# Kernel optimization log

Hardware: AMD Instinct MI355X
Metric: run time of the kernel (lower is better)

The kernel has to match this reference:

```python
import jax, jax.numpy as jnp
import numpy as np
from jax import lax

B, C_IN, C_OUT, N, R, K = 16, 64, 64, 32768, 32, 3
GROUPS, GN_EPS = 8, 1e-5


def swish(x):
    return x * jax.nn.sigmoid(x)


def group_norm(x, gamma, beta):
    b, c = x.shape[:2]
    xg = x.reshape(b, GROUPS, -1)
    mu = xg.mean(-1, keepdims=True)
    var = xg.var(-1, keepdims=True)
    xn = ((xg - mu) * lax.rsqrt(var + GN_EPS)).reshape(x.shape)
    shp = (1, c) + (1,) * (x.ndim - 2)
    return xn * gamma.reshape(shp) + beta.reshape(shp)


def conv3d(x, w, b):
    y = lax.conv_general_dilated(x, w, (1, 1, 1), 'SAME',
                                 dimension_numbers=('NCDHW', 'OIDHW', 'NCDHW'))
    return y + b.reshape(1, -1, 1, 1, 1)


def voxelize(features, coords):
    # features [B,C,N], coords [B,3,N] -> vox [B,C,R,R,R], norm_coords [B,3,N] in [0,R-1]
    c = coords - coords.mean(axis=2, keepdims=True)
    scale = jnp.linalg.norm(c, axis=1, keepdims=True).max(axis=2, keepdims=True) * 2.0  # eps=0
    norm = jnp.clip((c / scale + 0.5) * R, 0.0, R - 1)
    vc = jnp.round(norm).astype(jnp.int32)
    idx = (vc[:, 0] * R + vc[:, 1]) * R + vc[:, 2]  # [B,N] flat voxel index

    def per_batch(f, i):  # f [C,N], i [N] -> [C, R^3] scatter-average
        sums = jax.ops.segment_sum(f.T, i, num_segments=R ** 3)  # [R^3, C]
        cnt = jax.ops.segment_sum(jnp.ones(i.shape, f.dtype), i, num_segments=R ** 3)
        return (sums / jnp.maximum(cnt, 1.0)[:, None]).T

    vox = jax.vmap(per_batch)(features, idx).reshape(features.shape[0], features.shape[1], R, R, R)
    return vox, norm


def trilinear_devoxelize(vox, coords):
    # vox [B,C,R,R,R], coords [B,3,N] float in [0,R-1] -> [B,C,N]
    b, c = vox.shape[:2]
    flat = vox.reshape(b, c, R ** 3)
    c0f = jnp.floor(coords)
    f = coords - c0f
    i0 = jnp.clip(c0f.astype(jnp.int32), 0, R - 1)
    i1 = jnp.clip(i0 + 1, 0, R - 1)
    out = jnp.zeros((b, c, coords.shape[2]), vox.dtype)
    for xi, wx in ((i0[:, 0], 1.0 - f[:, 0]), (i1[:, 0], f[:, 0])):
        for yi, wy in ((i0[:, 1], 1.0 - f[:, 1]), (i1[:, 1], f[:, 1])):
            for zi, wz in ((i0[:, 2], 1.0 - f[:, 2]), (i1[:, 2], f[:, 2])):
                idx = (xi * R + yi) * R + zi  # [B,N]
                w = (wx * wy * wz)[:, None, :]
                out = out + jnp.take_along_axis(flat, idx[:, None, :], axis=2) * w
    return out


def setup_inputs():
    key = jax.random.key(0)
    ks = jax.random.split(key, 6)
    s1 = 1.0 / np.sqrt(C_IN * K ** 3)
    s2 = 1.0 / np.sqrt(C_OUT * K ** 3)
    sp = 1.0 / np.sqrt(C_IN)
    return {
        'features': jax.random.normal(ks[0], (B, C_IN, N), jnp.float32),
        'coords': jax.random.normal(ks[1], (B, 3, N), jnp.float32),
        'w1': jax.random.normal(ks[2], (C_OUT, C_IN, K, K, K), jnp.float32) * s1,
        'b1': jnp.zeros((C_OUT,), jnp.float32),
        'g1': jnp.ones((C_OUT,), jnp.float32),
        'be1': jnp.zeros((C_OUT,), jnp.float32),
        'w2': jax.random.normal(ks[3], (C_OUT, C_OUT, K, K, K), jnp.float32) * s2,
        'b2': jnp.zeros((C_OUT,), jnp.float32),
        'g2': jnp.ones((C_OUT,), jnp.float32),
        'be2': jnp.zeros((C_OUT,), jnp.float32),
        'wp': jax.random.normal(ks[4], (C_OUT, C_IN), jnp.float32) * sp,
        'bp': jnp.zeros((C_OUT,), jnp.float32),
        'gp': jnp.ones((C_OUT,), jnp.float32),
        'bep': jnp.zeros((C_OUT,), jnp.float32),
    }


def reference(features, coords, w1, b1, g1, be1, w2, b2, g2, be2, wp, bp, gp, bep):
    coords_sg = lax.stop_gradient(coords)  # torch: coords.detach() inside Voxelization
    vox, norm_coords = voxelize(features, coords_sg)
    h = swish(group_norm(conv3d(vox, w1, b1), g1, be1))
    # Dropout(0.1) is identity in eval mode
    h = swish(group_norm(conv3d(h, w2, b2), g2, be2))
    vpts = trilinear_devoxelize(h, norm_coords)
    pf = swish(group_norm(jnp.einsum('oc,bcn->bon', wp, features) + bp[None, :, None], gp, bep))
    return (vpts + pf, coords)
```

## Files before the change

kernel.cpp:

```cpp
#include <hip/hip_runtime.h>
#include <hip/hip_bf16.h>
#include <math.h>

#define BB   16
#define CCH  64
#define NPT  32768
#define RR   32
#define R3   32768
#define GSZ  262144
#define VOXB 2228224

typedef __attribute__((ext_vector_type(8))) short bfx8;
typedef __attribute__((ext_vector_type(8))) unsigned short usx8;
typedef __attribute__((ext_vector_type(16))) float f32x16;

__device__ __forceinline__ short f2bf(float f) {
    unsigned u = __builtin_bit_cast(unsigned, f);
    u += 0x7fff + ((u >> 16) & 1);
    return (short)(u >> 16);
}
__device__ __forceinline__ float bf2f(unsigned short s) {
    unsigned u = ((unsigned)s) << 16;
    return __builtin_bit_cast(float, u);
}

__device__ __forceinline__ int fzswz(int z) {
    return (((z & 3) ^ ((z >> 2) & 3)) << 3);
}

__device__ __forceinline__ float blockReduceSumF(float v) {
    __shared__ float sm[16];
    #pragma unroll
    for (int o = 32; o > 0; o >>= 1) v += __shfl_down(v, o);
    __syncthreads();
    if ((threadIdx.x & 63) == 0) sm[threadIdx.x >> 6] = v;
    __syncthreads();
    float s = 0.f;
    int nw = blockDim.x >> 6;
    for (int i = 0; i < nw; ++i) s += sm[i];
    return s;
}

__device__ __forceinline__ float blockReduceMaxF(float v) {
    __shared__ float sm[16];
    #pragma unroll
    for (int o = 32; o > 0; o >>= 1) v = fmaxf(v, __shfl_down(v, o));
    __syncthreads();
    if ((threadIdx.x & 63) == 0) sm[threadIdx.x >> 6] = v;
    __syncthreads();
    float s = sm[0];
    int nw = blockDim.x >> 6;
    for (int i = 1; i < nw; ++i) s = fmaxf(s, sm[i]);
    return s;
}

__global__ void k_cstat_sum(const float* __restrict__ coords, float* __restrict__ csum) {
    int b = blockIdx.x >> 3, seg = blockIdx.x & 7;
    const float* cb = coords + (size_t)b * 3 * NPT;
    int n0 = seg << 12;
    float sx = 0.f, sy = 0.f, sz = 0.f;
    for (int n = n0 + threadIdx.x; n < n0 + 4096; n += 256) {
        sx += cb[n]; sy += cb[NPT + n]; sz += cb[2 * NPT + n];
    }
    sx = blockReduceSumF(sx);
    sy = blockReduceSumF(sy);
    sz = blockReduceSumF(sz);
    if (threadIdx.x == 0) {
        atomicAdd(&csum[b * 4 + 0], sx);
        atomicAdd(&csum[b * 4 + 1], sy);
        atomicAdd(&csum[b * 4 + 2], sz);
    }
}

__global__ void k_cstat_max(const float* __restrict__ coords, const float* __restrict__ csum,
                            int* __restrict__ cmax) {
    int b = blockIdx.x >> 3, seg = blockIdx.x & 7;
    const float* cb = coords + (size_t)b * 3 * NPT;
    float mx = csum[b * 4 + 0] * (1.f / NPT);
    float my = csum[b * 4 + 1] * (1.f / NPT);
    float mz = csum[b * 4 + 2] * (1.f / NPT);
    int n0 = seg << 12;
    float mn = 0.f;
    for (int n = n0 + threadIdx.x; n < n0 + 4096; n += 256) {
        float x = cb[n] - mx, y = cb[NPT + n] - my, z = cb[2 * NPT + n] - mz;
        mn = fmaxf(mn, sqrtf(x * x + y * y + z * z));
    }
    mn = blockReduceMaxF(mn);
    if (threadIdx.x == 0) atomicMax(&cmax[b], __float_as_int(mn));
}

__global__ void k_norm_idx(const float* __restrict__ coords, const float* __restrict__ csum,
                           const int* __restrict__ cmax,
                           float* __restrict__ normc, int* __restrict__ vidx,
                           int* __restrict__ hist, float* __restrict__ out2) {
    int t = blockIdx.x * 256 + threadIdx.x;
    int b = t >> 15, n = t & 32767;
    float mx = csum[b * 4 + 0] * (1.f / NPT);
    float my = csum[b * 4 + 1] * (1.f / NPT);
    float mz = csum[b * 4 + 2] * (1.f / NPT);
    float scale = 2.f * __int_as_float(cmax[b]);
    const float* cb = coords + (size_t)b * 3 * NPT;
    float x = cb[n], y = cb[NPT + n], z = cb[2 * NPT + n];
    float nx = fminf(fmaxf(((x - mx) / scale + 0.5f) * 32.f, 0.f), 31.f);
    float ny = fminf(fmaxf(((y - my) / scale + 0.5f) * 32.f, 0.f), 31.f);
    float nz = fminf(fmaxf(((z - mz) / scale + 0.5f) * 32.f, 0.f), 31.f);
    float* nb = normc + (size_t)b * 3 * NPT;
    nb[n] = nx; nb[NPT + n] = ny; nb[2 * NPT + n] = nz;
    int vx = (int)rintf(nx), vy = (int)rintf(ny), vz = (int)rintf(nz);
    int v = (vx * 32 + vy) * 32 + vz;
    vidx[t] = v;
    atomicAdd(&hist[(b << 15) + v], 1);
    float* o2 = out2 + (size_t)b * 3 * NPT;
    o2[n] = x; o2[NPT + n] = y; o2[2 * NPT + n] = z;
}

__global__ __launch_bounds__(1024) void k_prefix(const int* __restrict__ hist,
                                                 int* __restrict__ startB,
                                                 int* __restrict__ base) {
    int b = blockIdx.x;
    int tid = threadIdx.x;
    const int* h = hist + (b << 15);
    int loc[32];
    int s = 0;
    #pragma unroll
    for (int j = 0; j < 32; ++j) { loc[j] = h[tid * 32 + j]; s += loc[j]; }
    __shared__ int sm[1024];
    sm[tid] = s;
    __syncthreads();
    for (int o = 1; o < 1024; o <<= 1) {
        int v = (tid >= o) ? sm[tid - o] : 0;
        __syncthreads();
        sm[tid] += v;
        __syncthreads();
    }
    int run = (tid ? sm[tid - 1] : 0);
    #pragma unroll
    for (int j = 0; j < 32; ++j) {
        int idx = (b << 15) + tid * 32 + j;
        startB[idx] = run;
        base[idx] = run;
        run += loc[j];
    }
}

__global__ __launch_bounds__(256) void k_reorder(const float* __restrict__ feat,
                                                 const int* __restrict__ vidx,
                                                 int* __restrict__ base,
                                                 short* __restrict__ featT) {
    __shared__ float tile[64][65];
    __shared__ int sslot[64];
    int blk = blockIdx.x;
    int b = blk >> 9;
    int n0 = (blk & 511) << 6;
    int tid = threadIdx.x;
    const float* fb = feat + ((size_t)b << 21);
    for (int e = tid; e < 64 * 16; e += 256) {
        int c = e >> 4, n4 = e & 15;
        float4 v4 = *(const float4*)(fb + ((size_t)c << 15) + n0 + n4 * 4);
        tile[c][n4 * 4 + 0] = v4.x; tile[c][n4 * 4 + 1] = v4.y;
        tile[c][n4 * 4 + 2] = v4.z; tile[c][n4 * 4 + 3] = v4.w;
    }
    if (tid < 64) {
        int v = vidx[(b << 15) + n0 + tid];
        sslot[tid] = atomicAdd(&base[(b << 15) + v], 1);
    }
    __syncthreads();
    int p = tid >> 2, q = tid & 3;
    int slot = sslot[p];
    short* dst = featT + (((size_t)((b << 15) + slot)) << 6) + q * 16;
    unsigned pk[8];
    #pragma unroll
    for (int k = 0; k < 8; ++k) {
        unsigned lo16 = (unsigned short)f2bf(tile[q * 16 + 2 * k][p]);
        unsigned hi16 = (unsigned short)f2bf(tile[q * 16 + 2 * k + 1][p]);
        pk[k] = lo16 | (hi16 << 16);
    }
    *(int4*)dst = make_int4(pk[0], pk[1], pk[2], pk[3]);
    *(int4*)(dst + 8) = make_int4(pk[4], pk[5], pk[6], pk[7]);
}

__global__ void k_vox_accum(const short* __restrict__ featT, const int* __restrict__ startB,
                            const int* __restrict__ base, short* __restrict__ vout) {
    int t = blockIdx.x * 256 + threadIdx.x;
    int lane4 = t & 15;
    int ph = (t >> 4) & 1;
    int v = (t >> 5) & 32767;
    int b = t >> 20;
    int start = startB[(b << 15) + v];
    int end   = base[(b << 15) + v];
    float4 acc = make_float4(0.f, 0.f, 0.f, 0.f);
    const short* fT = featT + (((size_t)b << 15) << 6) + lane4 * 4;
    for (int p = start + ph; p < end; p += 2) {
        short4 hv = *(const short4*)(fT + ((size_t)p << 6));
        acc.x += bf2f((unsigned short)hv.x);
        acc.y += bf2f((unsigned short)hv.y);
        acc.z += bf2f((unsigned short)hv.z);
        acc.w += bf2f((unsigned short)hv.w);
    }
    acc.x += __shfl_xor(acc.x, 16);
    acc.y += __shfl_xor(acc.y, 16);
    acc.z += __shfl_xor(acc.z, 16);
    acc.w += __shfl_xor(acc.w, 16);
    if (ph == 0) {
        float rc = 1.f / fmaxf((float)(end - start), 1.f);
        short4 pk;
        pk.x = f2bf(acc.x * rc); pk.y = f2bf(acc.y * rc);
        pk.z = f2bf(acc.z * rc); pk.w = f2bf(acc.w * rc);
        *(short4*)(vout + (size_t)b * VOXB + ((size_t)(v >> 5) * 34 + (v & 31) + 1) * 64 + lane4 * 4) = pk;
    }
}

__global__ void k_padzero(short* __restrict__ v) {
    int t = blockIdx.x * 256 + threadIdx.x;
    int q = t & 7, zp = (t >> 3) & 1, xy = (t >> 4) & 1023, b = t >> 14;
    int z = zp ? 33 : 0;
    *(int4*)(v + (size_t)b * VOXB + ((size_t)xy * 34 + z) * 64 + q * 8) = make_int4(0, 0, 0, 0);
}

__global__ void k_wprep2(const float* __restrict__ w1, const float* __restrict__ w2,
                         short* __restrict__ wT1, short* __restrict__ wT2) {
    int e = blockIdx.x * 256 + threadIdx.x;
    const float* w = (e < 110592) ? w1 : w2;
    short* o = (e < 110592) ? wT1 : wT2;
    int ee = (e < 110592) ? e : e - 110592;
    int ci = ee & 63, co = (ee >> 6) & 63, k = ee >> 12;
    o[ee] = f2bf(w[(size_t)(co * 64 + ci) * 27 + k]);
}

__global__ void k_gnprep(const float* __restrict__ st, const float* __restrict__ g,
                         const float* __restrict__ be,
                         float* __restrict__ scl, float* __restrict__ sft) {
    int t = blockIdx.x * 256 + threadIdx.x;
    int b = t >> 6, c = t & 63, cg = c >> 3;
    float s = st[(b * 8 + cg) * 2 + 0], s2 = st[(b * 8 + cg) * 2 + 1];
    float mean = s * (1.f / 262144.f);
    float rstd = rsqrtf(s2 * (1.f / 262144.f) - mean * mean + 1e-5f);
    float gm = g[c];
    scl[t] = gm * rstd;
    sft[t] = be[c] - mean * gm * rstd;
}

template<bool FUSE>
__global__ __launch_bounds__(512, 4) void k_conv_mfma(
    const short* __restrict__ vin, const short* __restrict__ wT,
    const float* __restrict__ bias,
    const float* __restrict__ scl, const float* __restrict__ sft,
    short* __restrict__ vout, float* __restrict__ st)
{
    __shared__ short lds[36 * 1088];
    __shared__ float sred[8][2];
    int bid = blockIdx.x;
    int xcd = bid & 7, sub = bid >> 3;
    int b = (xcd << 1) | (sub >> 6);
    int tile = sub & 63;
    int x0 = (tile >> 3) << 2, y0 = (tile & 7) << 2;
    int tid = threadIdx.x;
    int wv8 = tid >> 6;
    int cb = wv8 & 1, xl = wv8 >> 1;
    int l = tid & 63, lo = l & 31, hi = l >> 5;
    const short* vb = vin + (size_t)b * VOXB;
    int xo = x0 + xl;
    if (tid < 16) ((float*)sred)[tid] = 0.f;

    f32x16 acc[4];
    #pragma unroll
    for (int j = 0; j < 4; ++j)
        #pragma unroll
        for (int i = 0; i < 16; ++i) acc[j][i] = 0.f;

    #pragma unroll
    for (int h = 0; h < 2; ++h) {
        if (h) __syncthreads();
        #pragma unroll
        for (int it = 0; it < 9; ++it) {
            int e = it * 512 + tid;
            int line = e >> 7, r = e & 127;
            int z = r >> 2, q = r & 3;
            int xx = line / 6, yy = line - xx * 6;
            int xi = x0 + xx - 1, yi = y0 + yy - 1;
            bool inb = ((unsigned)xi < 32u) && ((unsigned)yi < 32u);
            int4 v = make_int4(0, 0, 0, 0);
            if (inb)
                v = *(const int4*)(vb + ((size_t)(xi * 32 + yi) * 34 + z) * 64 + h * 32 + q * 8);
            if (FUSE) {
                if (inb && z >= 1) {
                    int ci0 = (b << 6) + h * 32 + q * 8;
                    float4 sa = *(const float4*)(scl + ci0);
                    float4 sb = *(const float4*)(scl + ci0 + 4);
                    float4 fa = *(const float4*)(sft + ci0);
                    float4 fb = *(const float4*)(sft + ci0 + 4);
                    float sv[8] = {sa.x, sa.y, sa.z, sa.w, sb.x, sb.y, sb.z, sb.w};
                    float fv[8] = {fa.x, fa.y, fa.z, fa.w, fb.x, fb.y, fb.z, fb.w};
                    unsigned short* hv = (unsigned short*)&v;
                    #pragma unroll
                    for (int i = 0; i < 8; ++i) {
                        float g = fmaf(bf2f(hv[i]), sv[i], fv[i]);
                        float sw = g / (1.f + __expf(-g));
                        hv[i] = (unsigned short)f2bf(sw);
                    }
                }
            }
            int dst = line * 1088 + z * 32 + ((q * 8) ^ fzswz(z));
            *(int4*)(lds + dst) = v;
        }
        if (tid < 288) {
            int line = tid >> 3, rq = tid & 7;
            int z = 32 + (rq >> 2), q = rq & 3;
            int xx = line / 6, yy = line - xx * 6;
            int xi = x0 + xx - 1, yi = y0 + yy - 1;
            bool inb = ((unsigned)xi < 32u) && ((unsigned)yi < 32u);
            int4 v = make_int4(0, 0, 0, 0);
            if (inb)
                v = *(const int4*)(vb + ((size_t)(xi * 32 + yi) * 34 + z) * 64 + h * 32 + q * 8);
            if (FUSE) {
                if (inb && z <= 32) {
                    int ci0 = (b << 6) + h * 32 + q * 8;
                    float4 sa = *(const float4*)(scl + ci0);
                    float4 sb = *(const float4*)(scl + ci0 + 4);
                    float4 fa = *(const float4*)(sft + ci0);
                    float4 fb = *(const float4*)(sft + ci0 + 4);
                    float sv[8] = {sa.x, sa.y, sa.z, sa.w, sb.x, sb.y, sb.z, sb.w};
                    float fv[8] = {fa.x, fa.y, fa.z, fa.w, fb.x, fb.y, fb.z, fb.w};
                    unsigned short* hv = (unsigned short*)&v;
                    #pragma unroll
                    for (int i = 0; i < 8; ++i) {
                        float g = fmaf(bf2f(hv[i]), sv[i], fv[i]);
                        float sw = g / (1.f + __expf(-g));
                        hv[i] = (unsigned short)f2bf(sw);
                    }
                }
            }
            int dst = line * 1088 + z * 32 + ((q * 8) ^ fzswz(z));
            *(int4*)(lds + dst) = v;
        }
        __syncthreads();
        const short* wbase = wT + lo * 64 + h * 32 + hi * 8 + cb * 2048;
        #pragma unroll
        for (int dx = 0; dx < 3; ++dx) {
            const short* ldsx = lds + ((xl + dx) * 6) * 1088;
            #pragma unroll
            for (int dz = 0; dz < 3; ++dz) {
                int zz = lo + dz;
                int swz = fzswz(zz);
                const short* bcol = ldsx + zz * 32;
                #pragma unroll
                for (int s = 0; s < 2; ++s) {
                    int slot = (s * 16 + hi * 8) ^ swz;
                    const short* wt0 = wbase + (dx * 9 + dz) * 4096 + s * 16;
                    bfx8 w0 = *(const bfx8*)(wt0);
                    bfx8 w1 = *(const bfx8*)(wt0 + 3 * 4096);
                    bfx8 w2 = *(const bfx8*)(wt0 + 6 * 4096);
                    #pragma unroll
                    for (int L = 0; L < 6; ++L) {
                        bfx8 bv = *(const bfx8*)(bcol + L * 1088 + slot);
                        if (L <= 3)
                            acc[L] = __builtin_amdgcn_mfma_f32_32x32x16_bf16(w0, bv, acc[L], 0, 0, 0);
                        if (L >= 1 && L <= 4)
                            acc[L-1] = __builtin_amdgcn_mfma_f32_32x32x16_bf16(w1, bv, acc[L-1], 0, 0, 0);
                        if (L >= 2)
                            acc[L-2] = __builtin_amdgcn_mfma_f32_32x32x16_bf16(w2, bv, acc[L-2], 0, 0, 0);
                    }
                }
            }
        }
    }

    float gs[4], gs2[4];
    #pragma unroll
    for (int g = 0; g < 4; ++g) { gs[g] = 0.f; gs2[g] = 0.f; }
    short* ob = vout + (size_t)b * VOXB;
    #pragma unroll
    for (int j = 0; j < 4; ++j) {
        size_t rb = ((size_t)(xo * 32 + y0 + j) * 34 + 1 + lo) * 64;
        #pragma unroll
        for (int q = 0; q < 4; ++q) {
            int co0 = cb * 32 + hi * 4 + q * 8;
            float v0 = acc[j][q * 4 + 0] + bias[co0 + 0];
            float v1 = acc[j][q * 4 + 1] + bias[co0 + 1];
            float v2 = acc[j][q * 4 + 2] + bias[co0 + 2];
            float v3 = acc[j][q * 4 + 3] + bias[co0 + 3];
            gs[q] += v0 + v1 + v2 + v3;
            gs2[q] += v0 * v0 + v1 * v1 + v2 * v2 + v3 * v3;
            short4 pk;
            pk.x = f2bf(v0); pk.y = f2bf(v1); pk.z = f2bf(v2); pk.w = f2bf(v3);
            *(short4*)(ob + rb + co0) = pk;
        }
    }
    #pragma unroll
    for (int q = 0; q < 4; ++q) {
        float s = gs[q], s2 = gs2[q];
        #pragma unroll
        for (int o = 32; o > 0; o >>= 1) { s += __shfl_down(s, o); s2 += __shfl_down(s2, o); }
        if (l == 0) { atomicAdd(&sred[cb * 4 + q][0], s); atomicAdd(&sred[cb * 4 + q][1], s2); }
    }
    __syncthreads();
    if (tid < 8) {
        atomicAdd(&st[((b << 3) + tid) * 2 + 0], sred[tid][0]);
        atomicAdd(&st[((b << 3) + tid) * 2 + 1], sred[tid][1]);
    }
}

__global__ __launch_bounds__(256) void k_point(const float* __restrict__ feat,
                                               const float* __restrict__ wp,
                                               const float* __restrict__ bp,
                                               short* __restrict__ pbuf,
                                               float* __restrict__ stp) {
    __shared__ float s_f[64][64];
    __shared__ float s_w[64][68];
    __shared__ float sred[8][2];
    int nblk = blockIdx.x * 64;
    int b = blockIdx.y;
    int tid = threadIdx.x;
    if (tid < 16) ((float*)sred)[tid] = 0.f;
    const float* fb = feat + (((size_t)b * CCH) << 15);
    for (int e = tid; e < 64 * 64; e += 256) {
        int c = e >> 6, nn = e & 63;
        s_f[c][nn] = fb[(((size_t)c) << 15) + nblk + nn];
        s_w[nn][c] = wp[e];
    }
    __syncthreads();
    int o0 = (tid >> 4) << 2;
    int n0 = (tid & 15) << 2;
    float acc[4][4] = {{0.f}};
    for (int c = 0; c < 64; ++c) {
        float4 fv = *(const float4*)&s_f[c][n0];
        float4 wv = *(const float4*)&s_w[c][o0];
        float fvv[4] = {fv.x, fv.y, fv.z, fv.w};
        float wvv[4] = {wv.x, wv.y, wv.z, wv.w};
        #pragma unroll
        for (int j = 0; j < 4; ++j)
            #pragma unroll
            for (int i = 0; i < 4; ++i) acc[j][i] += wvv[j] * fvv[i];
    }
    float bb0 = bp[o0], bb1 = bp[o0 + 1], bb2 = bp[o0 + 2], bb3 = bp[o0 + 3];
    float s = 0.f, s2 = 0.f;
    #pragma unroll
    for (int i = 0; i < 4; ++i) {
        float v0 = acc[0][i] + bb0, v1 = acc[1][i] + bb1;
        float v2 = acc[2][i] + bb2, v3 = acc[3][i] + bb3;
        s += v0 + v1 + v2 + v3;
        s2 += v0 * v0 + v1 * v1 + v2 * v2 + v3 * v3;
        short4 pk;
        pk.x = f2bf(v0); pk.y = f2bf(v1); pk.z = f2bf(v2); pk.w = f2bf(v3);
        *(short4*)(pbuf + (((size_t)((b << 15) + nblk + n0 + i)) << 6) + o0) = pk;
    }
    int g = o0 >> 3;
    atomicAdd(&sred[g][0], s);
    atomicAdd(&sred[g][1], s2);
    __syncthreads();
    if (tid < 8) {
        atomicAdd(&stp[(b * 8 + tid) * 2 + 0], sred[tid][0]);
        atomicAdd(&stp[(b * 8 + tid) * 2 + 1], sred[tid][1]);
    }
}

__global__ __launch_bounds__(256) void k_final(
    const short* __restrict__ h, const float* __restrict__ normc,
    const float* __restrict__ scl2, const float* __restrict__ sft2,
    const float* __restrict__ stp, const float* __restrict__ gp,
    const float* __restrict__ bep, const short* __restrict__ pbuf,
    float* __restrict__ out1) {
    __shared__ float sm[64][33];
    int tid = threadIdx.x;
    int s = tid & 7, pp = tid >> 3;
    int blk = blockIdx.x;
    int b = blk >> 10;
    int n0 = (blk & 1023) << 5;
    int n = n0 + pp;
    const float* nb = normc + (size_t)b * 3 * NPT;
    float nx = nb[n], ny = nb[NPT + n], nz = nb[2 * NPT + n];
    float fxf = floorf(nx), fyf = floorf(ny), fzf = floorf(nz);
    float fx = nx - fxf, fy = ny - fyf, fz = nz - fzf;
    int x0 = (int)fxf; x0 = x0 < 31 ? x0 : 31;
    int y0 = (int)fyf; y0 = y0 < 31 ? y0 : 31;
    int z0 = (int)fzf; z0 = z0 < 31 ? z0 : 31;
    int x1 = x0 + 1 < 31 ? x0 + 1 : 31;
    int y1 = y0 + 1 < 31 ? y0 + 1 : 31;
    int z1 = z0 + 1 < 31 ? z0 + 1 : 31;
    float wx0 = 1.f - fx, wx1 = fx, wy0 = 1.f - fy, wy1 = fy, wz0 = 1.f - fz, wz1 = fz;

    float scl[8], sft[8];
    {
        int ci0 = (b << 6) + s * 8;
        float4 sa = *(const float4*)(scl2 + ci0);
        float4 sb = *(const float4*)(scl2 + ci0 + 4);
        float4 fa = *(const float4*)(sft2 + ci0);
        float4 fb = *(const float4*)(sft2 + ci0 + 4);
        scl[0] = sa.x; scl[1] = sa.y; scl[2] = sa.z; scl[3] = sa.w;
        scl[4] = sb.x; scl[5] = sb.y; scl[6] = sb.z; scl[7] = sb.w;
        sft[0] = fa.x; sft[1] = fa.y; sft[2] = fa.z; sft[3] = fa.w;
        sft[4] = fb.x; sft[5] = fb.y; sft[6] = fb.z; sft[7] = fb.w;
    }

    const short* hb = h + (size_t)b * VOXB + s * 8;
    float acc[8];
    #pragma unroll
    for (int i = 0; i < 8; ++i) acc[i] = 0.f;
    #pragma unroll
    for (int cx = 0; cx < 2; ++cx) {
        int xi = cx ? x1 : x0; float wxx = cx ? wx1 : wx0;
        #pragma unroll
        for (int cy = 0; cy < 2; ++cy) {
            int yi = cy ? y1 : y0; float wyy = cy ? wy1 : wy0;
            #pragma unroll
            for (int cz = 0; cz < 2; ++cz) {
                int zi = cz ? z1 : z0; float wzz = cz ? wz1 : wz0;
                float w = wxx * wyy * wzz;
                usx8 hv = *(const usx8*)(hb + ((size_t)(xi * 32 + yi) * 34 + zi + 1) * 64);
                #pragma unroll
                for (int i = 0; i < 8; ++i) {
                    float g = fmaf(bf2f(hv[i]), scl[i], sft[i]);
                    float sw = g / (1.f + __expf(-g));
                    acc[i] = fmaf(w, sw, acc[i]);
                }
            }
        }
    }
    float ss = stp[(b * 8 + s) * 2 + 0], ss2 = stp[(b * 8 + s) * 2 + 1];
    float mean = ss * (1.f / 262144.f);
    float rstd = rsqrtf(ss2 * (1.f / 262144.f) - mean * mean + 1e-5f);
    usx8 pv8 = *(const usx8*)(pbuf + (((size_t)((b << 15) + n)) << 6) + s * 8);
    #pragma unroll
    for (int i = 0; i < 8; ++i) {
        int co = s * 8 + i;
        float pv = bf2f(pv8[i]);
        float g = (pv - mean) * rstd * gp[co] + bep[co];
        float sw = g / (1.f + __expf(-g));
        sm[co][pp] = acc[i] + sw;
    }
    __syncthreads();
    int co = tid >> 2, q = (tid & 3) << 3;
    float r0 = sm[co][q + 0], r1 = sm[co][q + 1], r2 = sm[co][q + 2], r3 = sm[co][q + 3];
    float r4 = sm[co][q + 4], r5 = sm[co][q + 5], r6 = sm[co][q + 6], r7 = sm[co][q + 7];
    float* op = out1 + (((size_t)(b * CCH + co)) << 15) + n0 + q;
    *(float4*)op = make_float4(r0, r1, r2, r3);
    *(float4*)(op + 4) = make_float4(r4, r5, r6, r7);
}

extern "C" void kernel_launch(void* const* d_in, const int* in_sizes, int n_in,
                              void* d_out, int out_size, void* d_ws, size_t ws_size,
                              hipStream_t stream) {
    const float* feat   = (const float*)d_in[0];
    const float* coords = (const float*)d_in[1];
    const float* w1  = (const float*)d_in[2];
    const float* b1  = (const float*)d_in[3];
    const float* g1  = (const float*)d_in[4];
    const float* be1 = (const float*)d_in[5];
    const float* w2  = (const float*)d_in[6];
    const float* b2  = (const float*)d_in[7];
    const float* g2  = (const float*)d_in[8];
    const float* be2 = (const float*)d_in[9];
    const float* wp  = (const float*)d_in[10];
    const float* bp  = (const float*)d_in[11];
    const float* gp  = (const float*)d_in[12];
    const float* bep = (const float*)d_in[13];

    float* out1 = (float*)d_out;
    float* out2 = out1 + (size_t)BB * CCH * NPT;

    const size_t reg0Bytes = (size_t)BB * NPT * CCH * 4;
    short* featT    = (short*)d_ws;
    short* voxT_mid = (short*)d_ws;
    short* pbuf     = (short*)d_ws;
    short* voxT_in  = (short*)((char*)d_ws + reg0Bytes);
    char* p = (char*)voxT_in + (size_t)BB * VOXB * 2;
    int*   hist   = (int*)p;  p += (size_t)BB * R3 * 4;
    int*   startB = (int*)p;  p += (size_t)BB * R3 * 4;
    int*   base   = (int*)p;  p += (size_t)BB * R3 * 4;
    float* normc = (float*)p; p += (size_t)BB * 3 * NPT * 4;
    int*   vidx  = (int*)p;   p += (size_t)BB * NPT * 4;
    short* wT1   = (short*)p; p += 110592 * 2;
    short* wT2   = (short*)p; p += 110592 * 2;
    float* st1   = (float*)p; p += 256 * 4;
    float* st2   = (float*)p; p += 256 * 4;
    float* stp   = (float*)p; p += 256 * 4;
    float* csum  = (float*)p; p += 64 * 4;
    int*   cmax  = (int*)p;   p += 16 * 4;
    float* scl1  = (float*)p; p += 1024 * 4;
    float* sft1  = (float*)p; p += 1024 * 4;
    float* scl2  = (float*)p; p += 1024 * 4;
    float* sft2  = (float*)p; p += 1024 * 4;

    hipMemsetAsync(hist, 0, (size_t)BB * R3 * 4, stream);
    hipMemsetAsync(st1, 0, (256 * 3 + 64 + 16) * 4, stream);

    k_padzero<<<1024, 256, 0, stream>>>(voxT_in);
    k_cstat_sum<<<128, 256, 0, stream>>>(coords, csum);
    k_cstat_max<<<128, 256, 0, stream>>>(coords, csum, cmax);
    k_norm_idx<<<(BB * NPT) / 256, 256, 0, stream>>>(coords, csum, cmax, normc, vidx, hist, out2);
    k_prefix<<<BB, 1024, 0, stream>>>(hist, startB, base);
    k_reorder<<<(BB * NPT) / 64, 256, 0, stream>>>(feat, vidx, base, featT);
    k_vox_accum<<<(BB * R3 * 32) / 256, 256, 0, stream>>>(featT, startB, base, voxT_in);
    k_wprep2<<<864, 256, 0, stream>>>(w1, w2, wT1, wT2);

    k_padzero<<<1024, 256, 0, stream>>>(voxT_mid);

    k_conv_mfma<false><<<1024, 512, 0, stream>>>(voxT_in, wT1, b1,
                                                 nullptr, nullptr, voxT_mid, st1);
    k_gnprep<<<4, 256, 0, stream>>>(st1, g1, be1, scl1, sft1);
    k_conv_mfma<true><<<1024, 512, 0, stream>>>(voxT_mid, wT2, b2,
                                                scl1, sft1, voxT_in, st2);
    k_gnprep<<<4, 256, 0, stream>>>(st2, g2, be2, scl2, sft2);

    k_point<<<dim3(NPT / 64, BB), 256, 0, stream>>>(feat, wp, bp, pbuf, stp);

    k_final<<<(BB * NPT) / 32, 256, 0, stream>>>(voxT_in, normc, scl2, sft2,
                                                 stp, gp, bep, pbuf, out1);
}
```

Before: 737.5 us.

## Restructure conv waves to cover both channel halves, merge zeroing kernels

Result: slower. 764.1 us (+3.6%).

```diff
diff --git a/kernel.cpp b/kernel.cpp
--- a/kernel.cpp
+++ b/kernel.cpp
@@ -24,10 +24,6 @@
     return __builtin_bit_cast(float, u);
 }
 
-__device__ __forceinline__ int fzswz(int z) {
-    return (((z & 3) ^ ((z >> 2) & 3)) << 3);
-}
-
 __device__ __forceinline__ float blockReduceSumF(float v) {
     __shared__ float sm[16];
     #pragma unroll
@@ -52,6 +48,21 @@
     int nw = blockDim.x >> 6;
     for (int i = 1; i < nw; ++i) s = fmaxf(s, sm[i]);
     return s;
+}
+
+__global__ void k_zero(short* __restrict__ voxTin, int* __restrict__ hist,
+                       float* __restrict__ stblk) {
+    int t = blockIdx.x * 256 + threadIdx.x;
+    if (t < 262144) {
+        int q = t & 7, zp = (t >> 3) & 1, xy = (t >> 4) & 1023, b = t >> 14;
+        int z = zp ? 33 : 0;
+        *(int4*)(voxTin + (size_t)b * VOXB + ((size_t)xy * 34 + z) * 64 + q * 8) =
+            make_int4(0, 0, 0, 0);
+    } else if (t < 262144 + 131072) {
+        ((int4*)hist)[t - 262144] = make_int4(0, 0, 0, 0);
+    } else if (t < 262144 + 131072 + 212) {
+        ((int4*)stblk)[t - 262144 - 131072] = make_int4(0, 0, 0, 0);
+    }
 }
 
 __global__ void k_cstat_sum(const float* __restrict__ coords, float* __restrict__ csum) {
@@ -183,31 +194,24 @@
                             const int* __restrict__ base, short* __restrict__ vout) {
     int t = blockIdx.x * 256 + threadIdx.x;
     int lane4 = t & 15;
-    int ph = (t >> 4) & 1;
-    int v = (t >> 5) & 32767;
-    int b = t >> 20;
+    int v = (t >> 4) & 32767;
+    int b = t >> 19;
     int start = startB[(b << 15) + v];
     int end   = base[(b << 15) + v];
     float4 acc = make_float4(0.f, 0.f, 0.f, 0.f);
     const short* fT = featT + (((size_t)b << 15) << 6) + lane4 * 4;
-    for (int p = start + ph; p < end; p += 2) {
+    for (int p = start; p < end; ++p) {
         short4 hv = *(const short4*)(fT + ((size_t)p << 6));
         acc.x += bf2f((unsigned short)hv.x);
         acc.y += bf2f((unsigned short)hv.y);
         acc.z += bf2f((unsigned short)hv.z);
         acc.w += bf2f((unsigned short)hv.w);
     }
-    acc.x += __shfl_xor(acc.x, 16);
-    acc.y += __shfl_xor(acc.y, 16);
-    acc.z += __shfl_xor(acc.z, 16);
-    acc.w += __shfl_xor(acc.w, 16);
-    if (ph == 0) {
-        float rc = 1.f / fmaxf((float)(end - start), 1.f);
-        short4 pk;
-        pk.x = f2bf(acc.x * rc); pk.y = f2bf(acc.y * rc);
-        pk.z = f2bf(acc.z * rc); pk.w = f2bf(acc.w * rc);
-        *(short4*)(vout + (size_t)b * VOXB + ((size_t)(v >> 5) * 34 + (v & 31) + 1) * 64 + lane4 * 4) = pk;
-    }
+    float rc = 1.f / fmaxf((float)(end - start), 1.f);
+    short4 pk;
+    pk.x = f2bf(acc.x * rc); pk.y = f2bf(acc.y * rc);
+    pk.z = f2bf(acc.z * rc); pk.w = f2bf(acc.w * rc);
+    *(short4*)(vout + (size_t)b * VOXB + ((size_t)(v >> 5) * 34 + (v & 31) + 1) * 64 + lane4 * 4) = pk;
 }
 
 __global__ void k_padzero(short* __restrict__ v) {
@@ -241,7 +245,7 @@
 }
 
 template<bool FUSE>
-__global__ __launch_bounds__(512, 4) void k_conv_mfma(
+__global__ __launch_bounds__(256, 2) void k_conv_mfma(
     const short* __restrict__ vin, const short* __restrict__ wT,
     const float* __restrict__ bias,
     const float* __restrict__ scl, const float* __restrict__ sft,
@@ -255,25 +259,26 @@
     int tile = sub & 63;
     int x0 = (tile >> 3) << 2, y0 = (tile & 7) << 2;
     int tid = threadIdx.x;
-    int wv8 = tid >> 6;
-    int cb = wv8 & 1, xl = wv8 >> 1;
-    int l = tid & 63, lo = l & 31, hi = l >> 5;
+    int wv = tid >> 6, l = tid & 63;
+    int lo = l & 31, hi = l >> 5;
     const short* vb = vin + (size_t)b * VOXB;
-    int xo = x0 + xl;
+    int xo = x0 + wv;
     if (tid < 16) ((float*)sred)[tid] = 0.f;
 
-    f32x16 acc[4];
-    #pragma unroll
-    for (int j = 0; j < 4; ++j)
+    f32x16 acc[2][4];
+    #pragma unroll
+    for (int cb = 0; cb < 2; ++cb)
         #pragma unroll
-        for (int i = 0; i < 16; ++i) acc[j][i] = 0.f;
+        for (int j = 0; j < 4; ++j)
+            #pragma unroll
+            for (int i = 0; i < 16; ++i) acc[cb][j][i] = 0.f;
 
     #pragma unroll
     for (int h = 0; h < 2; ++h) {
         if (h) __syncthreads();
         #pragma unroll
-        for (int it = 0; it < 9; ++it) {
-            int e = it * 512 + tid;
+        for (int it = 0; it < 18; ++it) {
+            int e = it * 256 + tid;
             int line = e >> 7, r = e & 127;
             int z = r >> 2, q = r & 3;
             int xx = line / 6, yy = line - xx * 6;
@@ -300,11 +305,11 @@
                     }
                 }
             }
-            int dst = line * 1088 + z * 32 + ((q * 8) ^ fzswz(z));
+            int dst = line * 1088 + z * 32 + ((q * 8) ^ ((z & 3) << 3));
             *(int4*)(lds + dst) = v;
         }
-        if (tid < 288) {
-            int line = tid >> 3, rq = tid & 7;
+        for (int e2 = tid; e2 < 288; e2 += 256) {
+            int line = e2 >> 3, rq = e2 & 7;
             int z = 32 + (rq >> 2), q = rq & 3;
             int xx = line / 6, yy = line - xx * 6;
             int xi = x0 + xx - 1, yi = y0 + yy - 1;
@@ -330,68 +335,81 @@
                     }
                 }
             }
-            int dst = line * 1088 + z * 32 + ((q * 8) ^ fzswz(z));
+            int dst = line * 1088 + z * 32 + ((q * 8) ^ ((z & 3) << 3));
             *(int4*)(lds + dst) = v;
         }
         __syncthreads();
-        const short* wbase = wT + lo * 64 + h * 32 + hi * 8 + cb * 2048;
+        const short* wbase = wT + lo * 64 + h * 32 + hi * 8;
         #pragma unroll
         for (int dx = 0; dx < 3; ++dx) {
-            const short* ldsx = lds + ((xl + dx) * 6) * 1088;
+            const short* ldsx = lds + ((wv + dx) * 6) * 1088;
             #pragma unroll
             for (int dz = 0; dz < 3; ++dz) {
                 int zz = lo + dz;
-                int swz = fzswz(zz);
+                int swz = (zz & 3) << 3;
                 const short* bcol = ldsx + zz * 32;
                 #pragma unroll
                 for (int s = 0; s < 2; ++s) {
                     int slot = (s * 16 + hi * 8) ^ swz;
                     const short* wt0 = wbase + (dx * 9 + dz) * 4096 + s * 16;
-                    bfx8 w0 = *(const bfx8*)(wt0);
-                    bfx8 w1 = *(const bfx8*)(wt0 + 3 * 4096);
-                    bfx8 w2 = *(const bfx8*)(wt0 + 6 * 4096);
+                    bfx8 wA0 = *(const bfx8*)(wt0);
+                    bfx8 wB0 = *(const bfx8*)(wt0 + 2048);
+                    bfx8 wA1 = *(const bfx8*)(wt0 + 3 * 4096);
+                    bfx8 wB1 = *(const bfx8*)(wt0 + 3 * 4096 + 2048);
+                    bfx8 wA2 = *(const bfx8*)(wt0 + 6 * 4096);
+                    bfx8 wB2 = *(const bfx8*)(wt0 + 6 * 4096 + 2048);
                     #pragma unroll
                     for (int L = 0; L < 6; ++L) {
                         bfx8 bv = *(const bfx8*)(bcol + L * 1088 + slot);
-                        if (L <= 3)
-                            acc[L] = __builtin_amdgcn_mfma_f32_32x32x16_bf16(w0, bv, acc[L], 0, 0, 0);
-                        if (L >= 1 && L <= 4)
-                            acc[L-1] = __builtin_amdgcn_mfma_f32_32x32x16_bf16(w1, bv, acc[L-1], 0, 0, 0);
-                        if (L >= 2)
-                            acc[L-2] = __builtin_amdgcn_mfma_f32_32x32x16_bf16(w2, bv, acc[L-2], 0, 0, 0);
+                        if (L <= 3) {
+                            acc[0][L] = __builtin_amdgcn_mfma_f32_32x32x16_bf16(wA0, bv, acc[0][L], 0, 0, 0);
+                            acc[1][L] = __builtin_amdgcn_mfma_f32_32x32x16_bf16(wB0, bv, acc[1][L], 0, 0, 0);
+                        }
+                        if (L >= 1 && L <= 4) {
+                            acc[0][L-1] = __builtin_amdgcn_mfma_f32_32x32x16_bf16(wA1, bv, acc[0][L-1], 0, 0, 0);
+                            acc[1][L-1] = __builtin_amdgcn_mfma_f32_32x32x16_bf16(wB1, bv, acc[1][L-1], 0, 0, 0);
+                        }
+                        if (L >= 2) {
+                            acc[0][L-2] = __builtin_amdgcn_mfma_f32_32x32x16_bf16(wA2, bv, acc[0][L-2], 0, 0, 0);
+                            acc[1][L-2] = __builtin_amdgcn_mfma_f32_32x32x16_bf16(wB2, bv, acc[1][L-2], 0, 0, 0);
+                        }
                     }
                 }
             }
         }
     }
 
-    float gs[4], gs2[4];
-    #pragma unroll
-    for (int g = 0; g < 4; ++g) { gs[g] = 0.f; gs2[g] = 0.f; }
+    float gs[8], gs2[8];
+    #pragma unroll
+    for (int g = 0; g < 8; ++g) { gs[g] = 0.f; gs2[g] = 0.f; }
     short* ob = vout + (size_t)b * VOXB;
     #pragma unroll
-    for (int j = 0; j < 4; ++j) {
-        size_t rb = ((size_t)(xo * 32 + y0 + j) * 34 + 1 + lo) * 64;
+    for (int cb = 0; cb < 2; ++cb) {
         #pragma unroll
-        for (int q = 0; q < 4; ++q) {
-            int co0 = cb * 32 + hi * 4 + q * 8;
-            float v0 = acc[j][q * 4 + 0] + bias[co0 + 0];
-            float v1 = acc[j][q * 4 + 1] + bias[co0 + 1];
-            float v2 = acc[j][q * 4 + 2] + bias[co0 + 2];
-            float v3 = acc[j][q * 4 + 3] + bias[co0 + 3];
-            gs[q] += v0 + v1 + v2 + v3;
-            gs2[q] += v0 * v0 + v1 * v1 + v2 * v2 + v3 * v3;
-            short4 pk;
-            pk.x = f2bf(v0); pk.y = f2bf(v1); pk.z = f2bf(v2); pk.w = f2bf(v3);
-            *(short4*)(ob + rb + co0) = pk;
+        for (int j = 0; j < 4; ++j) {
+            size_t rb = ((size_t)(xo * 32 + y0 + j) * 34 + 1 + lo) * 64;
+            #pragma unroll
+            for (int q = 0; q < 4; ++q) {
+                int co0 = cb * 32 + hi * 4 + q * 8;
+                float v0 = acc[cb][j][q * 4 + 0] + bias[co0 + 0];
+                float v1 = acc[cb][j][q * 4 + 1] + bias[co0 + 1];
+                float v2 = acc[cb][j][q * 4 + 2] + bias[co0 + 2];
+                float v3 = acc[cb][j][q * 4 + 3] + bias[co0 + 3];
+                int g = cb * 4 + q;
+                gs[g] += v0 + v1 + v2 + v3;
+                gs2[g] += v0 * v0 + v1 * v1 + v2 * v2 + v3 * v3;
+                short4 pk;
+                pk.x = f2bf(v0); pk.y = f2bf(v1); pk.z = f2bf(v2); pk.w = f2bf(v3);
+                *(short4*)(ob + rb + co0) = pk;
+            }
         }
     }
     #pragma unroll
-    for (int q = 0; q < 4; ++q) {
-        float s = gs[q], s2 = gs2[q];
+    for (int g = 0; g < 8; ++g) {
+        float s = gs[g], s2 = gs2[g];
         #pragma unroll
         for (int o = 32; o > 0; o >>= 1) { s += __shfl_down(s, o); s2 += __shfl_down(s2, o); }
-        if (l == 0) { atomicAdd(&sred[cb * 4 + q][0], s); atomicAdd(&sred[cb * 4 + q][1], s2); }
+        if (l == 0) { atomicAdd(&sred[g][0], s); atomicAdd(&sred[g][1], s2); }
     }
     __syncthreads();
     if (tid < 8) {
@@ -581,24 +599,21 @@
     float* scl2  = (float*)p; p += 1024 * 4;
     float* sft2  = (float*)p; p += 1024 * 4;
 
-    hipMemsetAsync(hist, 0, (size_t)BB * R3 * 4, stream);
-    hipMemsetAsync(st1, 0, (256 * 3 + 64 + 16) * 4, stream);
-
-    k_padzero<<<1024, 256, 0, stream>>>(voxT_in);
+    k_zero<<<1537, 256, 0, stream>>>(voxT_in, hist, st1);
+    k_wprep2<<<864, 256, 0, stream>>>(w1, w2, wT1, wT2);
     k_cstat_sum<<<128, 256, 0, stream>>>(coords, csum);
     k_cstat_max<<<128, 256, 0, stream>>>(coords, csum, cmax);
     k_norm_idx<<<(BB * NPT) / 256, 256, 0, stream>>>(coords, csum, cmax, normc, vidx, hist, out2);
     k_prefix<<<BB, 1024, 0, stream>>>(hist, startB, base);
     k_reorder<<<(BB * NPT) / 64, 256, 0, stream>>>(feat, vidx, base, featT);
-    k_vox_accum<<<(BB * R3 * 32) / 256, 256, 0, stream>>>(featT, startB, base, voxT_in);
-    k_wprep2<<<864, 256, 0, stream>>>(w1, w2, wT1, wT2);
+    k_vox_accum<<<(BB * R3 * 16) / 256, 256, 0, stream>>>(featT, startB, base, voxT_in);
 
     k_padzero<<<1024, 256, 0, stream>>>(voxT_mid);
 
-    k_conv_mfma<false><<<1024, 512, 0, stream>>>(voxT_in, wT1, b1,
+    k_conv_mfma<false><<<1024, 256, 0, stream>>>(voxT_in, wT1, b1,
                                                  nullptr, nullptr, voxT_mid, st1);
     k_gnprep<<<4, 256, 0, stream>>>(st1, g1, be1, scl1, sft1);
-    k_conv_mfma<true><<<1024, 512, 0, stream>>>(voxT_mid, wT2, b2,
+    k_conv_mfma<true><<<1024, 256, 0, stream>>>(voxT_mid, wT2, b2,
                                                 scl1, sft1, voxT_in, st2);
     k_gnprep<<<4, 256, 0, stream>>>(st2, g2, be2, scl2, sft2);
 
```
